# Optimization experiments

Hardware: AMD Instinct MI355X
Metric: run time of the kernel (lower is better)

Reference implementation:

```python
import jax, jax.numpy as jnp
import numpy as np

B, S, D, H = 2, 2048, 1024, 16
HD = D // H  # head_dim = 64


def setup_inputs() -> dict:
    key = jax.random.key(0)
    ks = jax.random.split(key, 5)
    scale = 0.02
    x = jax.random.normal(ks[0], (B, S, D), dtype=jnp.float32)
    W_q = jax.random.normal(ks[1], (D, D), dtype=jnp.float32) * scale
    W_k = jax.random.normal(ks[2], (D, D), dtype=jnp.float32) * scale
    W_v = jax.random.normal(ks[3], (D, D), dtype=jnp.float32) * scale
    W_o = jax.random.normal(ks[4], (D, D), dtype=jnp.float32) * scale
    z = jnp.zeros((D,), dtype=jnp.float32)
    return {"x": x, "W_q": W_q, "b_q": z, "W_k": W_k, "b_k": z,
            "W_v": W_v, "b_v": z, "W_o": W_o, "b_o": z}


def _proj_heads(x, W, b):
    # [B,S,D] @ [D,D] -> [B,S,D] -> [B,H,S,HD]
    y = x @ W + b
    return y.reshape(x.shape[0], x.shape[1], H, HD).transpose(0, 2, 1, 3)


def reference(x, W_q, b_q, W_k, b_k, W_v, b_v, W_o, b_o):
    b, s, d = x.shape
    q = _proj_heads(x, W_q, b_q)  # [B,H,S,HD]
    k = _proj_heads(x, W_k, b_k)
    v = _proj_heads(x, W_v, b_v)
    scale = 1.0 / jnp.sqrt(jnp.float32(HD))
    # [B,H,S,S] causal scores
    scores = jnp.einsum('bhqe,bhke->bhqk', q, k) * scale
    causal = jnp.tril(jnp.ones((s, s), dtype=bool))
    scores = jnp.where(causal[None, None], scores, jnp.finfo(scores.dtype).min)
    attn = jax.nn.softmax(scores, axis=-1)
    ctx = jnp.einsum('bhqk,bhke->bhqe', attn, v)  # [B,H,S,HD]
    ctx = ctx.transpose(0, 2, 1, 3).reshape(b, s, d)
    return ctx @ W_o + b_o
```

## Files before the change

kernel.cpp:

```cpp
#include <hip/hip_runtime.h>
#include <hip/hip_bf16.h>
#include <math.h>


#define Bdim  2
#define Sdim  2048
#define Ddim  1024
#define Hn    16
#define HDdim 64
#define Mdim  (Bdim * Sdim)

#define QSCALE 0.18033688011112042f

typedef unsigned short ushort_t;
typedef __attribute__((ext_vector_type(8))) short bfrag;
typedef __attribute__((ext_vector_type(4))) float f4;

__device__ __forceinline__ ushort_t f2bf(float f) {
    union { float f; unsigned int i; } c;
    c.f = f;
    unsigned int x = c.i;
    unsigned int r = (x + 0x7fffu + ((x >> 16) & 1u)) >> 16;
    return (ushort_t)r;
}

__device__ __forceinline__ void glds16(const void* g, void* l) {
    __builtin_amdgcn_global_load_lds(
        (const __attribute__((address_space(1))) unsigned int*)g,
        (__attribute__((address_space(3))) unsigned int*)l, 16, 0, 0);
}

__global__ __launch_bounds__(256)
void cast_x(const float* __restrict__ x, ushort_t* __restrict__ xb)
{
    size_t i = ((size_t)blockIdx.x * 256 + threadIdx.x) * 8;
    float4 a = *(const float4*)(x + i);
    float4 b = *(const float4*)(x + i + 4);
    ushort_t o[8] = {f2bf(a.x), f2bf(a.y), f2bf(a.z), f2bf(a.w),
                     f2bf(b.x), f2bf(b.y), f2bf(b.z), f2bf(b.w)};
    *(bfrag*)(xb + i) = *(const bfrag*)o;
}

__global__ __launch_bounds__(256)
void wtrans(const float* __restrict__ W0, const float* __restrict__ W1,
            const float* __restrict__ W2, const float* __restrict__ W3,
            ushort_t* __restrict__ qkvT, ushort_t* __restrict__ oT)
{
    __shared__ ushort_t t[64][72];
    const int tid = threadIdx.x;
    const int z = blockIdx.z;
    const float* W = (z == 0) ? W0 : (z == 1) ? W1 : (z == 2) ? W2 : W3;
    const int k0 = blockIdx.y * 64, n0 = blockIdx.x * 64;

    const int r = tid >> 4, c4 = (tid & 15) * 4;
    #pragma unroll
    for (int rr = 0; rr < 4; ++rr) {
        int k = r + rr * 16;
        float4 v = *(const float4*)&W[(size_t)(k0 + k) * Ddim + n0 + c4];
        t[c4 + 0][k] = f2bf(v.x);
        t[c4 + 1][k] = f2bf(v.y);
        t[c4 + 2][k] = f2bf(v.z);
        t[c4 + 3][k] = f2bf(v.w);
    }
    __syncthreads();
    ushort_t* out = (z < 3) ? (qkvT + (size_t)z * Ddim * Ddim) : oT;
    const int n = tid >> 2, kc = (tid & 3) * 16;
    *(bfrag*)&out[(size_t)(n0 + n) * Ddim + k0 + kc] = *(const bfrag*)&t[n][kc];
    *(bfrag*)&out[(size_t)(n0 + n) * Ddim + k0 + kc + 8] = *(const bfrag*)&t[n][kc + 8];
}

template <int MODE>
__global__ __launch_bounds__(256)
void gemm_mfma(const ushort_t* __restrict__ A, const ushort_t* __restrict__ Bt,
               const float* __restrict__ bQ, const float* __restrict__ bK,
               const float* __restrict__ bV,
               ushort_t* __restrict__ oQ, ushort_t* __restrict__ oK,
               ushort_t* __restrict__ oVt, float* __restrict__ oF)
{
    __shared__ ushort_t As[128 * 32];
    __shared__ ushort_t Bs[128 * 32];

    const int tid  = threadIdx.x;
    const int lane = tid & 63;
    const int w    = tid >> 6;
    const int l15  = lane & 15;
    const int quad = lane >> 4;
    const int wr   = w >> 1, wc = w & 1;
    const int m0 = blockIdx.y * 128;
    const int n0 = blockIdx.x * 128;

    f4 acc[4][4];
    #pragma unroll
    for (int i = 0; i < 4; ++i)
        #pragma unroll
        for (int j = 0; j < 4; ++j) acc[i][j] = (f4){0.f, 0.f, 0.f, 0.f};

    const int srow  = w * 32 + (lane >> 2);
    const int selem = (lane & 3) * 8;
    const ushort_t* gA = A  + (size_t)(m0 + srow) * Ddim + selem;
    const ushort_t* gB = Bt + (size_t)(n0 + srow) * Ddim + selem;
    char* lA0 = (char*)As + (w * 32) * 64;
    char* lB0 = (char*)Bs + (w * 32) * 64;

    for (int kk = 0; kk < Ddim; kk += 32) {
        __syncthreads();
        glds16(gA + kk,              lA0);
        glds16(gA + 16 * Ddim + kk,  lA0 + 1024);
        glds16(gB + kk,              lB0);
        glds16(gB + 16 * Ddim + kk,  lB0 + 1024);
        __syncthreads();

        bfrag Af[4], Bf[4];
        #pragma unroll
        for (int i = 0; i < 4; ++i)
            Af[i] = *(const bfrag*)&As[(wr * 64 + i * 16 + l15) * 32 + quad * 8];
        #pragma unroll
        for (int j = 0; j < 4; ++j)
            Bf[j] = *(const bfrag*)&Bs[(wc * 64 + j * 16 + l15) * 32 + quad * 8];
        #pragma unroll
        for (int i = 0; i < 4; ++i)
            #pragma unroll
            for (int j = 0; j < 4; ++j)
                acc[i][j] = __builtin_amdgcn_mfma_f32_16x16x32_bf16(Af[i], Bf[j], acc[i][j], 0, 0, 0);
    }

    if constexpr (MODE == 0) {
        const int sel   = n0 >> 10;
        const int dbase = n0 & 1023;
        const float* bias = (sel == 0) ? bQ : (sel == 1) ? bK : bV;
        ushort_t* dst = (sel == 0) ? oQ : (sel == 1) ? oK : oVt;
        #pragma unroll
        for (int j = 0; j < 4; ++j) {
            int dn = dbase + wc * 64 + j * 16 + l15;
            float bv = bias[dn];
            int h = dn >> 6, e = dn & 63;
            #pragma unroll
            for (int i = 0; i < 4; ++i) {
                #pragma unroll
                for (int r = 0; r < 4; ++r) {
                    int m = m0 + wr * 64 + i * 16 + quad * 4 + r;
                    int b = m >> 11, s = m & 2047;
                    float v = acc[i][j][r] + bv;
                    if (sel == 0) v *= QSCALE;
                    if (sel < 2)
                        dst[((((size_t)b * Hn + h) * Sdim + s) << 6) + e] = f2bf(v);
                    else
                        dst[(((size_t)b * Hn + h) * HDdim + e) * Sdim + s] = f2bf(v);
                }
            }
        }
    } else {
        #pragma unroll
        for (int j = 0; j < 4; ++j) {
            int n = n0 + wc * 64 + j * 16 + l15;
            float bv = bQ[n];
            #pragma unroll
            for (int i = 0; i < 4; ++i)
                #pragma unroll
                for (int r = 0; r < 4; ++r) {
                    int m = m0 + wr * 64 + i * 16 + quad * 4 + r;
                    oF[(size_t)m * Ddim + n] = acc[i][j][r] + bv;
                }
        }
    }
}

#define NBH (Bdim * Hn)

#define MFMA16(a, b, c) __builtin_amdgcn_mfma_f32_16x16x32_bf16(a, b, c, 0, 0, 0)
#define EXP2(x) __builtin_amdgcn_exp2f(x)

__global__ __launch_bounds__(256, 4)
void flash_mfma(const ushort_t* __restrict__ Q, const ushort_t* __restrict__ K,
                const ushort_t* __restrict__ Vt, ushort_t* __restrict__ ctx)
{
    __shared__ ushort_t KtS[2][64 * 64];
    __shared__ ushort_t VsS[2][64 * 64];
    __shared__ ushort_t PTS[4][1024];

    const int tid  = threadIdx.x;
    const int lane = tid & 63;
    const int w    = tid >> 6;
    const int l15  = lane & 15;
    const int quad = lane >> 4;

    const int qb = 31 - (blockIdx.x >> 5);
    const int bh = blockIdx.x & 31;
    const int q0 = qb * 64;
    const int qw = q0 + w * 16;
    const int ntiles = qb + 1;

    const ushort_t* Qrow = Q + ((size_t)bh * Sdim + qw + l15) * HDdim;
    const bfrag Qf0 = *(const bfrag*)(Qrow + quad * 8);
    const bfrag Qf1 = *(const bfrag*)(Qrow + 32 + quad * 8);

    const ushort_t* Kp = K  + (size_t)bh * Sdim * HDdim;
    const ushort_t* Vp = Vt + (size_t)bh * HDdim * Sdim;

    const int srow = w * 8 + (lane >> 3);
    const int scol = ((lane & 7) ^ (lane >> 3)) * 8;
    const ushort_t* gK = Kp + (size_t)srow * HDdim + scol;
    const ushort_t* gV = Vp + (size_t)srow * Sdim + scol;
    char* ldsK = (char*)KtS + w * 1024;
    char* ldsV = (char*)VsS + w * 1024;
    ushort_t* PTw = PTS[w];

    const int sw = l15 & 7;
    const int c0 = (quad ^ sw) << 4;
    const int c1 = c0 ^ 64;
    const char* KtR = (const char*)KtS + l15 * 128;
    const char* VsR = (const char*)VsS + l15 * 128;

    f4 O[4];
    #pragma unroll
    for (int c = 0; c < 4; ++c) O[c] = (f4){0.f, 0.f, 0.f, 0.f};
    float m_prev = -INFINITY, l_run = 0.f;

    glds16(gK,                       ldsK);
    glds16(gK + 32 * HDdim,          ldsK + 4096);
    glds16(gV,                       ldsV);
    glds16(gV + (size_t)32 * Sdim,   ldsV + 4096);
    __syncthreads();

    for (int kt = 0; kt < ntiles - 1; ++kt) {
        const int k0  = kt << 6;
        const int buf = kt & 1;
        const int nb  = buf ^ 1;

        {
            const size_t kn = (size_t)(k0 + 64);
            glds16(gK + kn * HDdim,               ldsK + nb * 8192);
            glds16(gK + (kn + 32) * HDdim,        ldsK + nb * 8192 + 4096);
            glds16(gV + kn,                       ldsV + nb * 8192);
            glds16(gV + kn + (size_t)32 * Sdim,   ldsV + nb * 8192 + 4096);
        }

        const char* Kb = KtR + buf * 8192;
        const char* Vb = VsR + buf * 8192;

        float p[4][4];
        #pragma unroll
        for (int h = 0; h < 4; ++h) {
            bfrag a0 = *(const bfrag*)(Kb + h * 2048 + c0);
            bfrag a1 = *(const bfrag*)(Kb + h * 2048 + c1);
            f4 s = (f4){0.f, 0.f, 0.f, 0.f};
            s = MFMA16(a0, Qf0, s);
            s = MFMA16(a1, Qf1, s);
            #pragma unroll
            for (int r = 0; r < 4; ++r) p[h][r] = s[r];
        }

        float mh0 = fmaxf(fmaxf(p[0][0], p[0][1]), fmaxf(p[0][2], p[0][3]));
        float mh1 = fmaxf(fmaxf(p[1][0], p[1][1]), fmaxf(p[1][2], p[1][3]));
        float mh2 = fmaxf(fmaxf(p[2][0], p[2][1]), fmaxf(p[2][2], p[2][3]));
        float mh3 = fmaxf(fmaxf(p[3][0], p[3][1]), fmaxf(p[3][2], p[3][3]));
        float mt = fmaxf(fmaxf(mh0, mh1), fmaxf(mh2, mh3));
        mt = fmaxf(mt, __shfl_xor(mt, 16, 64));
        mt = fmaxf(mt, __shfl_xor(mt, 32, 64));

        if (__any(mt > m_prev + 8.f)) {
            float m_new = fmaxf(m_prev, mt);
            float alpha = EXP2(m_prev - m_new);
            l_run *= alpha;
            #pragma unroll
            for (int r = 0; r < 4; ++r) {
                float ar = __shfl(alpha, (lane & 48) + quad * 4 + r, 64);
                #pragma unroll
                for (int c = 0; c < 4; ++c) O[c][r] *= ar;
            }
            m_prev = m_new;
        }

        float rs0 = 0.f, rs1 = 0.f, rs2 = 0.f, rs3 = 0.f;
        #pragma unroll
        for (int r = 0; r < 4; ++r) {
            p[0][r] = EXP2(p[0][r] - m_prev); rs0 += p[0][r];
            p[1][r] = EXP2(p[1][r] - m_prev); rs1 += p[1][r];
            p[2][r] = EXP2(p[2][r] - m_prev); rs2 += p[2][r];
            p[3][r] = EXP2(p[3][r] - m_prev); rs3 += p[3][r];
        }
        float rsum = (rs0 + rs1) + (rs2 + rs3);
        rsum += __shfl_xor(rsum, 16, 64);
        rsum += __shfl_xor(rsum, 32, 64);
        l_run += rsum;

        #pragma unroll
        for (int h = 0; h < 4; ++h) {
            ushort_t pk[4] = {f2bf(p[h][0]), f2bf(p[h][1]),
                              f2bf(p[h][2]), f2bf(p[h][3])};
            *(uint2*)&PTw[((((h << 1) + (quad >> 1)) * 16 + l15) << 3) + (quad & 1) * 4] =
                *(const uint2*)pk;
        }
        bfrag pA0 = *(const bfrag*)&PTw[lane * 8];
        bfrag pA1 = *(const bfrag*)&PTw[512 + lane * 8];

        #pragma unroll
        for (int c = 0; c < 4; ++c) {
            bfrag v0 = *(const bfrag*)(Vb + c * 2048 + c0);
            bfrag v1 = *(const bfrag*)(Vb + c * 2048 + c1);
            O[c] = MFMA16(pA0, v0, O[c]);
            O[c] = MFMA16(pA1, v1, O[c]);
        }

        __syncthreads();
    }

    {
        const int buf = (ntiles - 1) & 1;
        const char* Kb = KtR + buf * 8192;
        const char* Vb = VsR + buf * 8192;

        float p[4][4];
        float mt = -INFINITY;
        #pragma unroll
        for (int h = 0; h < 4; ++h) {
            if (h <= w) {
                bfrag a0 = *(const bfrag*)(Kb + h * 2048 + c0);
                bfrag a1 = *(const bfrag*)(Kb + h * 2048 + c1);
                f4 s = (f4){0.f, 0.f, 0.f, 0.f};
                s = MFMA16(a0, Qf0, s);
                s = MFMA16(a1, Qf1, s);
                if (h == w) {
                    #pragma unroll
                    for (int r = 0; r < 4; ++r) {
                        float v = (quad * 4 + r <= l15) ? s[r] : -INFINITY;
                        p[h][r] = v;
                        mt = fmaxf(mt, v);
                    }
                } else {
                    #pragma unroll
                    for (int r = 0; r < 4; ++r) {
                        p[h][r] = s[r];
                        mt = fmaxf(mt, s[r]);
                    }
                }
            } else {
                #pragma unroll
                for (int r = 0; r < 4; ++r) p[h][r] = -INFINITY;
            }
        }
        mt = fmaxf(mt, __shfl_xor(mt, 16, 64));
        mt = fmaxf(mt, __shfl_xor(mt, 32, 64));

        if (__any(mt > m_prev + 8.f)) {
            float m_new = fmaxf(m_prev, mt);
            float alpha = EXP2(m_prev - m_new);
            l_run *= alpha;
            #pragma unroll
            for (int r = 0; r < 4; ++r) {
                float ar = __shfl(alpha, (lane & 48) + quad * 4 + r, 64);
                #pragma unroll
                for (int c = 0; c < 4; ++c) O[c][r] *= ar;
            }
            m_prev = m_new;
        }

        float rsum = 0.f;
        #pragma unroll
        for (int h = 0; h < 4; ++h)
            #pragma unroll
            for (int r = 0; r < 4; ++r) {
                float e = EXP2(p[h][r] - m_prev);
                p[h][r] = e;
                rsum += e;
            }
        rsum += __shfl_xor(rsum, 16, 64);
        rsum += __shfl_xor(rsum, 32, 64);
        l_run += rsum;

        #pragma unroll
        for (int h = 0; h < 4; ++h) {
            ushort_t pk[4] = {f2bf(p[h][0]), f2bf(p[h][1]),
                              f2bf(p[h][2]), f2bf(p[h][3])};
            *(uint2*)&PTw[((((h << 1) + (quad >> 1)) * 16 + l15) << 3) + (quad & 1) * 4] =
                *(const uint2*)pk;
        }
        bfrag pA0 = *(const bfrag*)&PTw[lane * 8];
        #pragma unroll
        for (int c = 0; c < 4; ++c) {
            bfrag v0 = *(const bfrag*)(Vb + c * 2048 + c0);
            O[c] = MFMA16(pA0, v0, O[c]);
        }
        if (w >= 2) {
            bfrag pA1 = *(const bfrag*)&PTw[512 + lane * 8];
            #pragma unroll
            for (int c = 0; c < 4; ++c) {
                bfrag v1 = *(const bfrag*)(Vb + c * 2048 + c1);
                O[c] = MFMA16(pA1, v1, O[c]);
            }
        }
    }

    const int b = bh >> 4, h = bh & 15;
    #pragma unroll
    for (int r = 0; r < 4; ++r) {
        float inv_l = 1.0f / __shfl(l_run, (lane & 48) + quad * 4 + r, 64);
        size_t base = ((size_t)b * Sdim + qw + quad * 4 + r) * Ddim + h * HDdim + l15;
        #pragma unroll
        for (int c = 0; c < 4; ++c)
            ctx[base + c * 16] = f2bf(O[c][r] * inv_l);
    }
}

extern "C" void kernel_launch(void* const* d_in, const int* in_sizes, int n_in,
                              void* d_out, int out_size, void* d_ws, size_t ws_size,
                              hipStream_t stream)
{
    const int NX = Mdim * Ddim;
    const int NW = Ddim * Ddim;
    int xi = 0, wi[4] = {1, 3, 5, 7}, bi[4] = {2, 4, 6, 8}, nw = 0, nb = 0;
    bool sized = true;
    for (int i = 0; i < 9; ++i) {
        if (in_sizes[i] == NX) xi = i;
        else if (in_sizes[i] == NW) { if (nw < 4) wi[nw++] = i; }
        else if (in_sizes[i] == Ddim) { if (nb < 4) bi[nb++] = i; }
        else sized = false;
    }
    int iWq, iWk, iWv, iWo, ibq, ibk, ibv, ibo;
    if (!sized || xi == 0) {
        xi = 0; iWq = 1; ibq = 2; iWk = 3; ibk = 4; iWv = 5; ibv = 6; iWo = 7; ibo = 8;
    } else {
        iWk = wi[0]; iWo = wi[1]; iWq = wi[2]; iWv = wi[3];
        ibk = bi[0]; ibo = bi[1]; ibq = bi[2]; ibv = bi[3];
    }

    const float* x  = (const float*)d_in[xi];
    const float* Wq = (const float*)d_in[iWq];
    const float* bq = (const float*)d_in[ibq];
    const float* Wk = (const float*)d_in[iWk];
    const float* bk = (const float*)d_in[ibk];
    const float* Wv = (const float*)d_in[iWv];
    const float* bv = (const float*)d_in[ibv];
    const float* Wo = (const float*)d_in[iWo];
    const float* bo = (const float*)d_in[ibo];
    float* out = (float*)d_out;

    const size_t elems = (size_t)Mdim * Ddim;
    const size_t welems = (size_t)Ddim * Ddim;
    ushort_t* Qb    = (ushort_t*)d_ws;
    ushort_t* Kb    = Qb + elems;
    ushort_t* Vtb   = Kb + elems;
    ushort_t* Cb    = Vtb + elems;
    ushort_t* xb    = Cb + elems;
    ushort_t* qkvT  = xb + elems;
    ushort_t* WoT   = qkvT + 3 * welems;

    dim3 blk(256);
    cast_x<<<dim3(Mdim * Ddim / (256 * 8)), blk, 0, stream>>>(x, xb);
    wtrans<<<dim3(16, 16, 4), blk, 0, stream>>>(Wq, Wk, Wv, Wo, qkvT, WoT);

    gemm_mfma<0><<<dim3(3 * Ddim / 128, Mdim / 128), blk, 0, stream>>>(
        xb, qkvT, bq, bk, bv, Qb, Kb, Vtb, nullptr);

    flash_mfma<<<dim3(32 * NBH), blk, 0, stream>>>(Qb, Kb, Vtb, Cb);

    gemm_mfma<1><<<dim3(Ddim / 128, Mdim / 128), blk, 0, stream>>>(
        Cb, WoT, bo, nullptr, nullptr, nullptr, nullptr, nullptr, out);
}
```

Measured before the change: 198.7 us.

## Merge prep kernels and use packed bf16 conversion in attention and V store

Folds the x cast and the weight transpose into one launch by adding extra z-slices to the grid, which saves a kernel launch. The flash-attention P tile now uses the v_cvt_pk_bf16_f32 instruction to convert pairs of floats instead of manual rounding. The transposed V store in the QKV GEMM writes two packed bf16 values per 32-bit store. The packed instruction's rounding mode may differ slightly from the hand-written round-to-nearest-even, and the cast blocks in the merged kernel reserve shared memory they never use.

```diff
diff --git a/kernel.cpp b/kernel.cpp
--- a/kernel.cpp
+++ b/kernel.cpp
@@ -24,6 +24,12 @@
     return (ushort_t)r;
 }
 
+__device__ __forceinline__ unsigned cvtpk(float lo, float hi) {
+    unsigned r;
+    asm("v_cvt_pk_bf16_f32 %0, %1, %2" : "=v"(r) : "v"(lo), "v"(hi));
+    return r;
+}
+
 __device__ __forceinline__ void glds16(const void* g, void* l) {
     __builtin_amdgcn_global_load_lds(
         (const __attribute__((address_space(1))) unsigned int*)g,
@@ -31,24 +37,26 @@
 }
 
 __global__ __launch_bounds__(256)
-void cast_x(const float* __restrict__ x, ushort_t* __restrict__ xb)
-{
-    size_t i = ((size_t)blockIdx.x * 256 + threadIdx.x) * 8;
-    float4 a = *(const float4*)(x + i);
-    float4 b = *(const float4*)(x + i + 4);
-    ushort_t o[8] = {f2bf(a.x), f2bf(a.y), f2bf(a.z), f2bf(a.w),
-                     f2bf(b.x), f2bf(b.y), f2bf(b.z), f2bf(b.w)};
-    *(bfrag*)(xb + i) = *(const bfrag*)o;
-}
-
-__global__ __launch_bounds__(256)
-void wtrans(const float* __restrict__ W0, const float* __restrict__ W1,
-            const float* __restrict__ W2, const float* __restrict__ W3,
-            ushort_t* __restrict__ qkvT, ushort_t* __restrict__ oT)
+void prep(const float* __restrict__ x, ushort_t* __restrict__ xb,
+          const float* __restrict__ W0, const float* __restrict__ W1,
+          const float* __restrict__ W2, const float* __restrict__ W3,
+          ushort_t* __restrict__ qkvT, ushort_t* __restrict__ oT)
 {
     __shared__ ushort_t t[64][72];
     const int tid = threadIdx.x;
     const int z = blockIdx.z;
+
+    if (z >= 4) {
+        size_t blk = (size_t)(z - 4) * 256 + blockIdx.y * 16 + blockIdx.x;
+        size_t i = (blk * 256 + tid) * 8;
+        float4 a = *(const float4*)(x + i);
+        float4 b = *(const float4*)(x + i + 4);
+        ushort_t o[8] = {f2bf(a.x), f2bf(a.y), f2bf(a.z), f2bf(a.w),
+                         f2bf(b.x), f2bf(b.y), f2bf(b.z), f2bf(b.w)};
+        *(bfrag*)(xb + i) = *(const bfrag*)o;
+        return;
+    }
+
     const float* W = (z == 0) ? W0 : (z == 1) ? W1 : (z == 2) ? W2 : W3;
     const int k0 = blockIdx.y * 64, n0 = blockIdx.x * 64;
 
@@ -134,18 +142,29 @@
             int dn = dbase + wc * 64 + j * 16 + l15;
             float bv = bias[dn];
             int h = dn >> 6, e = dn & 63;
-            #pragma unroll
-            for (int i = 0; i < 4; ++i) {
-                #pragma unroll
-                for (int r = 0; r < 4; ++r) {
-                    int m = m0 + wr * 64 + i * 16 + quad * 4 + r;
-                    int b = m >> 11, s = m & 2047;
-                    float v = acc[i][j][r] + bv;
-                    if (sel == 0) v *= QSCALE;
-                    if (sel < 2)
+            if (sel < 2) {
+                #pragma unroll
+                for (int i = 0; i < 4; ++i) {
+                    #pragma unroll
+                    for (int r = 0; r < 4; ++r) {
+                        int m = m0 + wr * 64 + i * 16 + quad * 4 + r;
+                        int b = m >> 11, s = m & 2047;
+                        float v = acc[i][j][r] + bv;
+                        if (sel == 0) v *= QSCALE;
                         dst[((((size_t)b * Hn + h) * Sdim + s) << 6) + e] = f2bf(v);
-                    else
-                        dst[(((size_t)b * Hn + h) * HDdim + e) * Sdim + s] = f2bf(v);
+                    }
+                }
+            } else {
+                #pragma unroll
+                for (int i = 0; i < 4; ++i) {
+                    #pragma unroll
+                    for (int rp = 0; rp < 2; ++rp) {
+                        int m = m0 + wr * 64 + i * 16 + quad * 4 + rp * 2;
+                        int b = m >> 11, s = m & 2047;
+                        unsigned pv = cvtpk(acc[i][j][rp * 2] + bv,
+                                            acc[i][j][rp * 2 + 1] + bv);
+                        *(unsigned*)&dst[(((size_t)b * Hn + h) * HDdim + e) * Sdim + s] = pv;
+                    }
                 }
             }
         }
@@ -286,10 +305,10 @@
 
         #pragma unroll
         for (int h = 0; h < 4; ++h) {
-            ushort_t pk[4] = {f2bf(p[h][0]), f2bf(p[h][1]),
-                              f2bf(p[h][2]), f2bf(p[h][3])};
-            *(uint2*)&PTw[((((h << 1) + (quad >> 1)) * 16 + l15) << 3) + (quad & 1) * 4] =
-                *(const uint2*)pk;
+            uint2 pw;
+            pw.x = cvtpk(p[h][0], p[h][1]);
+            pw.y = cvtpk(p[h][2], p[h][3]);
+            *(uint2*)&PTw[((((h << 1) + (quad >> 1)) * 16 + l15) << 3) + (quad & 1) * 4] = pw;
         }
         bfrag pA0 = *(const bfrag*)&PTw[lane * 8];
         bfrag pA1 = *(const bfrag*)&PTw[512 + lane * 8];
@@ -370,10 +389,10 @@
 
         #pragma unroll
         for (int h = 0; h < 4; ++h) {
-            ushort_t pk[4] = {f2bf(p[h][0]), f2bf(p[h][1]),
-                              f2bf(p[h][2]), f2bf(p[h][3])};
-            *(uint2*)&PTw[((((h << 1) + (quad >> 1)) * 16 + l15) << 3) + (quad & 1) * 4] =
-                *(const uint2*)pk;
+            uint2 pw;
+            pw.x = cvtpk(p[h][0], p[h][1]);
+            pw.y = cvtpk(p[h][2], p[h][3]);
+            *(uint2*)&PTw[((((h << 1) + (quad >> 1)) * 16 + l15) << 3) + (quad & 1) * 4] = pw;
         }
         bfrag pA0 = *(const bfrag*)&PTw[lane * 8];
         #pragma unroll
@@ -446,8 +465,7 @@
     ushort_t* WoT   = qkvT + 3 * welems;
 
     dim3 blk(256);
-    cast_x<<<dim3(Mdim * Ddim / (256 * 8)), blk, 0, stream>>>(x, xb);
-    wtrans<<<dim3(16, 16, 4), blk, 0, stream>>>(Wq, Wk, Wv, Wo, qkvT, WoT);
+    prep<<<dim3(16, 16, 12), blk, 0, stream>>>(x, xb, Wq, Wk, Wv, Wo, qkvT, WoT);
 
     gemm_mfma<0><<<dim3(3 * Ddim / 128, Mdim / 128), blk, 0, stream>>>(
         xb, qkvT, bq, bk, bv, Qb, Kb, Vtb, nullptr);
```

Result: faster. 189.2 us (-4.8%).
